# Optimization experiments

Hardware: AMD Instinct MI355X
Metric: run time of the kernel (lower is better)

The kernel has to match this reference:

```python
import jax, jax.numpy as jnp
import numpy as np

B, S, H, I, E, TOP_K, NS = 2, 2048, 2048, 1408, 8, 2, 2
SI = I * NS  # shared expert intermediate (intermediate_size * num_shared_expert)
INIT = 0.02


def setup_inputs() -> dict:
    key = jax.random.key(0)
    ks = jax.random.split(key, 9)
    f32 = jnp.float32
    return {
        "hidden_states": jax.random.normal(ks[0], (B, S, H), f32),
        # router classifier: Linear(H, E, bias=False), torch weight [E, H]
        "router_w": (jax.random.normal(ks[1], (E, H), f32) * INIT),
        # grouped experts (SwiGLU, no bias): [E, H, I], [E, H, I], [E, I, H]
        "gate_w": (jax.random.normal(ks[2], (E, H, I), f32) * INIT),
        "up_w": (jax.random.normal(ks[3], (E, H, I), f32) * INIT),
        "down_w": (jax.random.normal(ks[4], (E, I, H), f32) * INIT),
        # shared expert _MLP (bias=True), stored in matmul orientation
        "s_gate_w": (jax.random.normal(ks[5], (H, SI), f32) * INIT),
        "s_gate_b": jnp.zeros((SI,), f32),
        "s_up_w": (jax.random.normal(ks[6], (H, SI), f32) * INIT),
        "s_up_b": jnp.zeros((SI,), f32),
        "s_down_w": (jax.random.normal(ks[7], (SI, H), f32) * INIT),
        "s_down_b": jnp.zeros((H,), f32),
    }


def reference(hidden_states, router_w, gate_w, up_w, down_w,
              s_gate_w, s_gate_b, s_up_w, s_up_b, s_down_w, s_down_b):
    b, s, h = hidden_states.shape
    x = hidden_states.reshape(-1, h)          # [T, H]
    T = x.shape[0]
    num_experts = router_w.shape[0]

    # ---- router: logits -> fp32 softmax -> top-k -> renormalize ----
    logits = x @ router_w.T                   # [T, E]
    probs = jax.nn.softmax(logits.astype(jnp.float32), axis=-1)
    topk_w, topk_idx = jax.lax.top_k(probs, TOP_K)            # [T, K]
    topk_w = topk_w / jnp.sum(topk_w, axis=-1, keepdims=True)
    # dense combine weights [T, E]; zero for unrouted experts
    combine = jnp.zeros((T, num_experts), probs.dtype)
    combine = combine.at[jnp.arange(T)[:, None], topk_idx].add(topk_w)

    # ---- grouped SwiGLU experts; scan over E keeps peak memory at [T, I] ----
    def expert_step(acc, ws):
        gw, uw, dw, ce = ws                  # [H,I], [H,I], [I,H], [T]
        out = (jax.nn.silu(x @ gw) * (x @ uw)) @ dw           # [T, H]
        return acc + ce[:, None].astype(out.dtype) * out, None

    moe_out, _ = jax.lax.scan(expert_step, jnp.zeros_like(x),
                              (gate_w, up_w, down_w, combine.T))

    # ---- shared expert SwiGLU MLP (bias=True), overlapped -> added ----
    shared = (jax.nn.silu(x @ s_gate_w + s_gate_b)
              * (x @ s_up_w + s_up_b)) @ s_down_w + s_down_b

    return (moe_out + shared).reshape(b, s, h)
```

## Files before the change

### kernel.cpp

```cpp
#include <hip/hip_runtime.h>
#include <hip/hip_bf16.h>
#include <stdint.h>

#define T_TOK 4096
#define HDIM  2048
#define IDIM  1408
#define NEXP  8
#define SIDIM 2816
#define GU_CAP 781
#define DN_CAP 568

typedef __bf16 bf16_t;
typedef __bf16 bf16x8 __attribute__((ext_vector_type(8)));
typedef __bf16 bf16x4 __attribute__((ext_vector_type(4)));
typedef float  f32x4  __attribute__((ext_vector_type(4)));

typedef uint32_t __attribute__((address_space(3))) lds_u32;
typedef uint32_t __attribute__((address_space(1))) glb_u32;

__device__ __forceinline__ void glds16(const bf16_t* g, const char* l) {
  __builtin_amdgcn_global_load_lds((const glb_u32*)g, (lds_u32*)l, 16, 0, 0);
}

__device__ __forceinline__ void bar() {
  asm volatile("" ::: "memory");
  __builtin_amdgcn_s_barrier();
  asm volatile("" ::: "memory");
}
#define VMW4 asm volatile("s_waitcnt vmcnt(4)" ::: "memory")
#define VMW0 asm volatile("s_waitcnt vmcnt(0)" ::: "memory")

__device__ __forceinline__ int xcd_swz(int orig, int nwg) {
  int q = nwg >> 3, r = nwg & 7;
  int x = orig & 7, i = orig >> 3;
  return (x < r ? x * (q + 1) : r * (q + 1) + (x - r) * q) + i;
}

__global__ void tcvt_all_kernel(const float* __restrict__ gate, const float* __restrict__ up,
                                const float* __restrict__ sgw, const float* __restrict__ suw,
                                const float* __restrict__ down, const float* __restrict__ sdw,
                                bf16_t* __restrict__ BguR, bf16_t* __restrict__ BguS,
                                bf16_t* __restrict__ dT, bf16_t* __restrict__ sdT) {
  const int b = blockIdx.x;
  const float* in; bf16_t* out; int R, C, bx, by, which = 0; bool gu;
  if (b < 11264) {
    int z = b / 704, rem = b - z * 704;
    bx = rem % 22; by = rem / 22;
    int e = z >> 1; which = z & 1;
    in = (which ? up : gate) + (size_t)e * HDIM * IDIM;
    out = BguR + (size_t)e * (2 * IDIM) * HDIM;
    R = HDIM; C = IDIM; gu = true;
  } else if (b < 14080) {
    int k = b - 11264;
    int z = k / 1408, rem = k - z * 1408;
    bx = rem % 44; by = rem / 44;
    which = z;
    in = which ? suw : sgw;
    out = BguS;
    R = HDIM; C = SIDIM; gu = true;
  } else if (b < 19712) {
    int k = b - 14080;
    int z = k / 704, rem = k - z * 704;
    bx = rem % 32; by = rem / 32;
    in = down + (size_t)z * IDIM * HDIM;
    out = dT + (size_t)z * HDIM * IDIM;
    R = IDIM; C = HDIM; gu = false;
  } else {
    int k = b - 19712;
    bx = k % 32; by = k / 32;
    in = sdw; out = sdT;
    R = SIDIM; C = HDIM; gu = false;
  }
  __shared__ float tf[64 * 64];
  const int r0 = by * 64, c0 = bx * 64;
  const int tid = threadIdx.x;
  const int cb = tid & 15, rr = tid >> 4;
#pragma unroll
  for (int s = 0; s < 4; ++s) {
    int r = rr + 16 * s;
    float4 v = *(const float4*)(in + (size_t)(r0 + r) * C + c0 + cb * 4);
    int slot = (cb ^ (r & 7) ^ ((r >> 4) << 1)) & 15;
    *(float4*)&tf[r * 64 + slot * 4] = v;
  }
  __syncthreads();
  const int c = tid >> 2, rb = (tid & 3) * 16;
  bf16x8 w0, w1;
#pragma unroll
  for (int i = 0; i < 16; ++i) {
    int r = rb + i;
    int slot = ((c >> 2) ^ (r & 7) ^ ((r >> 4) << 1)) & 15;
    float v = tf[r * 64 + slot * 4 + (c & 3)];
    if (i < 8) w0[i] = (bf16_t)v; else w1[i - 8] = (bf16_t)v;
  }
  int cg = c0 + c;
  int nprime = gu ? (((cg >> 4) << 5) + which * 16 + (cg & 15)) : cg;
  bf16_t* op = out + (size_t)nprime * R + r0 + rb;
  *(bf16x8*)op = w0;
  *(bf16x8*)(op + 8) = w1;
}

__global__ void router_kernel(const float* __restrict__ x, const float* __restrict__ rw,
                              bf16_t* __restrict__ xb,
                              int* __restrict__ tk_i, float* __restrict__ tk_w,
                              int* __restrict__ counts) {
  int gtid = blockIdx.x * 256 + threadIdx.x;
  int t = gtid >> 6, lane = gtid & 63;
  const float4* xr = (const float4*)(x + (size_t)t * HDIM);
  bf16x4* xo = (bf16x4*)(xb + (size_t)t * HDIM);
  float acc[NEXP];
#pragma unroll
  for (int e = 0; e < NEXP; e++) acc[e] = 0.f;
  for (int i = lane; i < HDIM / 4; i += 64) {
    float4 xv = xr[i];
    bf16x4 o;
    o[0] = (bf16_t)xv.x; o[1] = (bf16_t)xv.y; o[2] = (bf16_t)xv.z; o[3] = (bf16_t)xv.w;
    xo[i] = o;
#pragma unroll
    for (int e = 0; e < NEXP; e++) {
      float4 wv = ((const float4*)(rw + e * HDIM))[i];
      acc[e] += xv.x * wv.x + xv.y * wv.y + xv.z * wv.z + xv.w * wv.w;
    }
  }
#pragma unroll
  for (int e = 0; e < NEXP; e++)
#pragma unroll
    for (int off = 32; off; off >>= 1) acc[e] += __shfl_down(acc[e], off);
  if (lane == 0) {
    int i1 = 0; float m1 = acc[0];
#pragma unroll
    for (int e = 1; e < NEXP; e++) if (acc[e] > m1) { m1 = acc[e]; i1 = e; }
    int i2 = -1; float m2 = -1e30f;
#pragma unroll
    for (int e = 0; e < NEXP; e++) if (e != i1 && acc[e] > m2) { m2 = acc[e]; i2 = e; }
    float w1 = 1.f / (1.f + __expf(m2 - m1));
    tk_i[t * 2] = i1; tk_i[t * 2 + 1] = i2;
    tk_w[t * 2] = w1; tk_w[t * 2 + 1] = 1.f - w1;
    atomicAdd(&counts[i1], 1); atomicAdd(&counts[i2], 1);
  }
}

__global__ void build_kernel(int* __restrict__ meta) {
  __shared__ int snmt;
  if (threadIdx.x == 0) {
    int o = 0;
    for (int e = 0; e < NEXP; e++) { meta[16 + e] = o; o += meta[e]; }
    meta[24] = o;
    int nmt = 0;
    for (int e = 0; e < NEXP; e++) {
      int nt = (meta[e] + 255) >> 8;
      for (int i = 0; i < nt; i++) { meta[32 + nmt] = e; meta[80 + nmt] = i << 8; nmt++; }
    }
    meta[25] = nmt;
    meta[26] = nmt * 11 + 352;
    meta[27] = nmt * 8 + 256;
    snmt = nmt;
  }
  __syncthreads();
  const int nmt = snmt;
  int4* gt = (int4*)(meta + 128);
  const int ng = nmt * 11 + 352;
  for (int i = threadIdx.x; i < ng; i += 256) {
    int4 v; v.w = 0;
    if (i < nmt * 11) {
      int g = i / (nmt * 2), rem = i - g * (nmt * 2);
      int yt, xt;
      if (g < 5) { yt = rem >> 1; xt = g * 2 + (rem & 1); }
      else       { yt = rem;      xt = 10; }
      v.x = 0 | (meta[32 + yt] << 1); v.y = meta[80 + yt]; v.z = xt * 256;
    } else {
      int k = i - nmt * 11;
      int g = k >> 5, rem = k & 31;
      int yt = rem >> 1, xt = g * 2 + (rem & 1);
      v.x = 1; v.y = yt * 256; v.z = xt * 256;
    }
    gt[i] = v;
  }
  int4* dt4 = (int4*)(meta + 3328);
  const int nd = nmt * 8 + 256;
  for (int i = threadIdx.x; i < nd; i += 256) {
    int4 v; v.w = 0;
    if (i < nmt * 8) {
      int g = i / (nmt * 2), rem = i - g * (nmt * 2);
      int yt = rem >> 1, xt = g * 2 + (rem & 1);
      v.x = 0 | (meta[32 + yt] << 1); v.y = meta[80 + yt]; v.z = xt * 256;
    } else {
      int k = i - nmt * 8;
      int xt = k >> 5, rem = k & 31, ks = rem >> 4, yt = rem & 15;
      v.x = 1 | (ks << 4); v.y = yt * 256; v.z = xt * 256;
    }
    dt4[i] = v;
  }
}

__global__ void scatter_kernel(const int* __restrict__ tk_i, const float* __restrict__ tk_w,
                               int* __restrict__ meta, int* __restrict__ tok_idx,
                               int* __restrict__ tk_slot) {
  int t = blockIdx.x * 256 + threadIdx.x;
  if (t >= T_TOK) return;
#pragma unroll
  for (int k = 0; k < 2; k++) {
    int e = tk_i[t * 2 + k];
    int pos = meta[16 + e] + atomicAdd(&meta[8 + e], 1);
    tok_idx[pos] = t; tk_slot[t * 2 + k] = pos;
  }
}

template <int OP>
__device__ __forceinline__
void gemm8p_body(const bf16_t* __restrict__ A0, const bf16_t* __restrict__ A1,
                 const bf16_t* __restrict__ B0, const bf16_t* __restrict__ B1,
                 bf16_t* __restrict__ O0, bf16_t* __restrict__ O1, bf16_t* __restrict__ O2,
                 const float* __restrict__ bg, const float* __restrict__ bu,
                 const int* __restrict__ meta, const int* __restrict__ tok_idx) {
  const int ntiles = meta[OP == 0 ? 26 : 27];
  const int l = blockIdx.x;
  if (l >= ntiles) return;
  const int s = xcd_swz(l, ntiles);
  const int4 tv = ((const int4*)(meta + (OP == 0 ? 128 : 3328)))[s];
  const int kind = tv.x & 1, e = (tv.x >> 1) & 7, ks = (tv.x >> 4) & 1;
  const int row0 = tv.y, n0 = tv.z;

  int cnt, slot0 = 0, strideA, strideB, koff = 0;
  const bf16_t *Ab, *Bp;
  constexpr int NKT = (OP == 0) ? (HDIM / 64) : (IDIM / 64);
  if (OP == 0) {
    strideA = HDIM; strideB = HDIM; Ab = A0;
    if (kind == 0) {
      slot0 = meta[16 + e]; cnt = meta[17 + e] - slot0;
      Bp = B0 + (size_t)e * (2 * IDIM) * HDIM;
    } else { cnt = T_TOK; Bp = B1; }
  } else {
    if (kind == 0) {
      slot0 = meta[16 + e]; cnt = meta[17 + e] - slot0;
      Ab = A0; strideA = IDIM;
      Bp = B0 + (size_t)e * HDIM * IDIM; strideB = IDIM;
    } else {
      cnt = T_TOK; Ab = A1; strideA = SIDIM;
      Bp = B1; strideB = SIDIM; koff = ks * IDIM;
    }
  }

  __shared__ __align__(16) char smem[131072];

  const int t = threadIdx.x;
  const int lane = t & 63, wid = t >> 6;
  const int wr = wid >> 2, wc = wid & 3;
  const int lr = lane & 15, lg = lane >> 4;

  const bf16_t* pA[4]; const bf16_t* pB[4]; int dG[4];
#pragma unroll
  for (int j = 0; j < 4; ++j) {
    int g = j * 512 + t;
    int r = g >> 3;
    int c16 = (g & 7) ^ (r & 7);
    dG[j] = g * 16;
    int rr = row0 + r;
    if (kind == 0 && rr >= cnt) rr = cnt - 1;
    int arow;
    if (OP == 0 && kind == 0) arow = tok_idx[slot0 + rr];
    else if (OP == 1 && kind == 0) arow = slot0 + rr;
    else arow = rr;
    pA[j] = Ab + (size_t)arow * strideA + koff + c16 * 8;
    pB[j] = Bp + (size_t)(n0 + r) * strideB + koff + c16 * 8;
  }

  const int cswz0 = ((lg) ^ (lr & 7)) * 16;
  const int cswz1 = ((4 + lg) ^ (lr & 7)) * 16;
  const int aRowB = (wr * 128 + lr) * 128;
  const int bRowB = (wc * 64 + lr) * 128 + 65536;

  f32x4 acc[8][4];
#pragma unroll
  for (int mi = 0; mi < 8; ++mi)
#pragma unroll
    for (int ni = 0; ni < 4; ++ni) acc[mi][ni] = (f32x4)(0.f);

  bf16x8 aL[4][2], aH[4][2], bL[2][2], bH[2][2];

#define ST_A(BUFO, KT, JH) { \
    glds16(pA[(JH)*2]   + (KT)*64, smem + (BUFO) + dG[(JH)*2]); \
    glds16(pA[(JH)*2+1] + (KT)*64, smem + (BUFO) + dG[(JH)*2+1]); }
#define ST_B(BUFO, KT, JH) { \
    glds16(pB[(JH)*2]   + (KT)*64, smem + 65536 + (BUFO) + dG[(JH)*2]); \
    glds16(pB[(JH)*2+1] + (KT)*64, smem + 65536 + (BUFO) + dG[(JH)*2+1]); }
#define RD_A(af, BUFO, MIH) { \
    _Pragma("unroll") for (int mi = 0; mi < 4; ++mi) { \
      af[mi][0] = *(const bf16x8*)(smem + (BUFO) + aRowB + (MIH)*8192 + mi*2048 + cswz0); \
      af[mi][1] = *(const bf16x8*)(smem + (BUFO) + aRowB + (MIH)*8192 + mi*2048 + cswz1); } }
#define RD_B(bf, BUFO, NIH) { \
    _Pragma("unroll") for (int ni = 0; ni < 2; ++ni) { \
      bf[ni][0] = *(const bf16x8*)(smem + (BUFO) + bRowB + (NIH)*4096 + ni*2048 + cswz0); \
      bf[ni][1] = *(const bf16x8*)(smem + (BUFO) + bRowB + (NIH)*4096 + ni*2048 + cswz1); } }
#define MMQ(af, bf, MO, NO) { \
    __builtin_amdgcn_s_setprio(1); \
    _Pragma("unroll") for (int ni = 0; ni < 2; ++ni) \
    _Pragma("unroll") for (int mi = 0; mi < 4; ++mi) { \
      acc[(MO)+mi][(NO)+ni] = __builtin_amdgcn_mfma_f32_16x16x32_bf16(af[mi][0], bf[ni][0], acc[(MO)+mi][(NO)+ni], 0, 0, 0); \
      acc[(MO)+mi][(NO)+ni] = __builtin_amdgcn_mfma_f32_16x16x32_bf16(af[mi][1], bf[ni][1], acc[(MO)+mi][(NO)+ni], 0, 0, 0); } \
    __builtin_amdgcn_s_setprio(0); }
#define KTILE(KT, BO, NBO, W) { \
    RD_A(aL, BO, 0); RD_B(bL, BO, 0); \
    if ((KT) + 1 < NKT) ST_B(NBO, (KT) + 1, 0); \
    bar(); MMQ(aL, bL, 0, 0); bar(); \
    RD_A(aH, BO, 1); \
    if ((KT) + 1 < NKT) ST_B(NBO, (KT) + 1, 1); \
    bar(); MMQ(aH, bL, 4, 0); bar(); \
    RD_B(bH, BO, 1); \
    if ((KT) + 2 < NKT) ST_A(BO, (KT) + 2, 0); \
    bar(); MMQ(aH, bH, 4, 2); bar(); \
    if ((KT) + 2 < NKT) ST_A(BO, (KT) + 2, 1); \
    bar(); MMQ(aL, bH, 0, 2); \
    W; bar(); }

  ST_A(0, 0, 0); ST_A(0, 0, 1);
  ST_B(0, 0, 0); ST_B(0, 0, 1);
  ST_A(32768, 1, 0); ST_A(32768, 1, 1);
  VMW4; bar();

  for (int kt = 0; kt < NKT - 2; kt += 2) {
    KTILE(kt, 0, 32768, VMW4);
    KTILE(kt + 1, 32768, 0, VMW4);
  }
  KTILE(NKT - 2, 0, 32768, VMW0);
  KTILE(NKT - 1, 32768, 0, VMW0);

  if (OP == 0) {
    bf16_t* Ho = kind ? O1 : O0;
    const int HN = kind ? SIDIM : IDIM;
    const int Lbase = n0 >> 1;
#pragma unroll
    for (int mi = 0; mi < 8; ++mi)
#pragma unroll
      for (int j = 0; j < 4; ++j) {
        int row = wr * 128 + mi * 16 + lg * 4 + j;
        int grow = row0 + row;
        if (kind == 0 && grow >= cnt) continue;
        size_t orow = (size_t)((kind ? 0 : slot0) + grow);
#pragma unroll
        for (int nih = 0; nih < 2; ++nih) {
          int Lr = wc * 32 + nih * 16 + lr;
          float g = acc[mi][2 * nih][j];
          float u = acc[mi][2 * nih + 1][j];
          if (kind) { g += bg[Lbase + Lr]; u += bu[Lbase + Lr]; }
          float h = (g / (1.f + __expf(-g))) * u;
          Ho[orow * HN + Lbase + Lr] = (bf16_t)h;
        }
      }
  } else {
    bf16_t* Po = kind ? (ks ? O2 : O1) : O0;
#pragma unroll
    for (int mi = 0; mi < 8; ++mi)
#pragma unroll
      for (int j = 0; j < 4; ++j) {
        int row = wr * 128 + mi * 16 + lg * 4 + j;
        int grow = row0 + row;
        if (kind == 0 && grow >= cnt) continue;
        size_t orow = (size_t)((kind ? 0 : slot0) + grow);
#pragma unroll
        for (int ni = 0; ni < 4; ++ni) {
          int col = n0 + wc * 64 + ni * 16 + lr;
          Po[orow * HDIM + col] = (bf16_t)acc[mi][ni][j];
        }
      }
  }
#undef ST_A
#undef ST_B
#undef RD_A
#undef RD_B
#undef MMQ
#undef KTILE
}

__global__ __launch_bounds__(512, 2)
void gu_gemm(const bf16_t* A0, const bf16_t* A1, const bf16_t* B0, const bf16_t* B1,
             bf16_t* O0, bf16_t* O1, bf16_t* O2, const float* bg, const float* bu,
             const int* meta, const int* tok_idx) {
  gemm8p_body<0>(A0, A1, B0, B1, O0, O1, O2, bg, bu, meta, tok_idx);
}
__global__ __launch_bounds__(512, 2)
void dn_gemm(const bf16_t* A0, const bf16_t* A1, const bf16_t* B0, const bf16_t* B1,
             bf16_t* O0, bf16_t* O1, bf16_t* O2, const float* bg, const float* bu,
             const int* meta, const int* tok_idx) {
  gemm8p_body<1>(A0, A1, B0, B1, O0, O1, O2, bg, bu, meta, tok_idx);
}

__global__ void combine_kernel(const bf16_t* __restrict__ sh0, const bf16_t* __restrict__ sh1,
                               const bf16_t* __restrict__ rt, const int* __restrict__ tk_slot,
                               const float* __restrict__ tk_w, const float* __restrict__ sdb,
                               float* __restrict__ out) {
  const int t = blockIdx.x;
  const int c = threadIdx.x * 8;
  const int s1 = tk_slot[2 * t], s2 = tk_slot[2 * t + 1];
  const float w1 = tk_w[2 * t], w2 = tk_w[2 * t + 1];
  bf16x8 a = *(const bf16x8*)(sh0 + (size_t)t * HDIM + c);
  bf16x8 b = *(const bf16x8*)(sh1 + (size_t)t * HDIM + c);
  bf16x8 r1 = *(const bf16x8*)(rt + (size_t)s1 * HDIM + c);
  bf16x8 r2 = *(const bf16x8*)(rt + (size_t)s2 * HDIM + c);
  float4 d0 = *(const float4*)(sdb + c);
  float4 d1 = *(const float4*)(sdb + c + 4);
  float o[8];
#pragma unroll
  for (int i = 0; i < 8; i++)
    o[i] = (float)a[i] + (float)b[i] + w1 * (float)r1[i] + w2 * (float)r2[i];
  o[0] += d0.x; o[1] += d0.y; o[2] += d0.z; o[3] += d0.w;
  o[4] += d1.x; o[5] += d1.y; o[6] += d1.z; o[7] += d1.w;
  float4* op = (float4*)(out + (size_t)t * HDIM + c);
  op[0] = make_float4(o[0], o[1], o[2], o[3]);
  op[1] = make_float4(o[4], o[5], o[6], o[7]);
}

extern "C" void kernel_launch(void* const* d_in, const int* in_sizes, int n_in,
                              void* d_out, int out_size, void* d_ws, size_t ws_size,
                              hipStream_t stream) {
  const float* x_f  = (const float*)d_in[0];
  const float* rw   = (const float*)d_in[1];
  const float* gate = (const float*)d_in[2];
  const float* up   = (const float*)d_in[3];
  const float* down = (const float*)d_in[4];
  const float* sgw  = (const float*)d_in[5];
  const float* sgb  = (const float*)d_in[6];
  const float* suw  = (const float*)d_in[7];
  const float* sub  = (const float*)d_in[8];
  const float* sdw  = (const float*)d_in[9];
  const float* sdb  = (const float*)d_in[10];
  float* out = (float*)d_out;

  char* ws = (char*)d_ws;
  size_t off = 0;
  auto alloc = [&](size_t bytes) {
    char* p = ws + off;
    off += (bytes + 255) & ~(size_t)255;
    return p;
  };
  bf16_t* xb    = (bf16_t*)alloc((size_t)T_TOK * HDIM * 2);
  char*   bgur  = alloc((size_t)NEXP * 2 * IDIM * HDIM * 2);
  bf16_t* BguR  = (bf16_t*)bgur;
  bf16_t* BguS  = (bf16_t*)alloc((size_t)2 * SIDIM * HDIM * 2);
  bf16_t* dT    = (bf16_t*)alloc((size_t)NEXP * HDIM * IDIM * 2);
  bf16_t* sdT   = (bf16_t*)alloc((size_t)HDIM * SIDIM * 2);
  bf16_t* hid_r = (bf16_t*)alloc((size_t)(T_TOK * 2) * IDIM * 2);
  bf16_t* hid_s = (bf16_t*)alloc((size_t)T_TOK * SIDIM * 2);
  int*    meta  = (int*)alloc(32768);
  int*    tok_idx = (int*)alloc(8192 * 4);
  int*    tk_slot = (int*)alloc(8192 * 4);
  int*    tk_i    = (int*)alloc((size_t)T_TOK * 2 * 4);
  float*  tk_w2   = (float*)alloc((size_t)T_TOK * 2 * 4);

  bf16_t* rt_p  = (bf16_t*)bgur;
  bf16_t* sh_p0 = (bf16_t*)(bgur + (size_t)8192 * HDIM * 2);
  bf16_t* sh_p1 = (bf16_t*)(bgur + (size_t)8192 * HDIM * 2 + (size_t)T_TOK * HDIM * 2);

  hipMemsetAsync(meta, 0, 64, stream);

  tcvt_all_kernel<<<21120, 256, 0, stream>>>(
      gate, up, sgw, suw, down, sdw, BguR, BguS, dT, sdT);

  router_kernel<<<T_TOK / 4, 256, 0, stream>>>(x_f, rw, xb, tk_i, tk_w2, meta);
  build_kernel<<<1, 256, 0, stream>>>(meta);
  scatter_kernel<<<T_TOK / 256, 256, 0, stream>>>(tk_i, tk_w2, meta, tok_idx, tk_slot);

  gu_gemm<<<GU_CAP, 512, 0, stream>>>(
      xb, nullptr, BguR, BguS, hid_r, hid_s, nullptr, sgb, sub, meta, tok_idx);
  dn_gemm<<<DN_CAP, 512, 0, stream>>>(
      hid_r, hid_s, dT, sdT, rt_p, sh_p0, sh_p1, nullptr, nullptr, meta, nullptr);
  combine_kernel<<<T_TOK, 256, 0, stream>>>(sh_p0, sh_p1, rt_p, tk_slot, tk_w2, sdb, out);
}
```

Measured before the change: 588.3 us.

## Drop build kernel; derive tile schedule from expert counts inside GEMM and scatter kernels

Removes the single-block build_kernel launch. Each GEMM block now recomputes per-expert offsets and tile counts from the raw counts and decodes its own tile descriptor, and scatter computes prefix offsets in shared memory. This saves one serialized launch and the table writes and reads, in exchange for a little redundant scalar work per block. It also adds an lgkmcnt(8) wait before the first barrier in the K-tile loop to order the LDS reads.

Result: faster. 567.9 us (-3.5%).

```diff
diff --git a/kernel.cpp b/kernel.cpp
--- a/kernel.cpp
+++ b/kernel.cpp
@@ -29,6 +29,7 @@
 }
 #define VMW4 asm volatile("s_waitcnt vmcnt(4)" ::: "memory")
 #define VMW0 asm volatile("s_waitcnt vmcnt(0)" ::: "memory")
+#define LGK8 asm volatile("s_waitcnt lgkmcnt(8)" ::: "memory")
 
 __device__ __forceinline__ int xcd_swz(int orig, int nwg) {
   int q = nwg >> 3, r = nwg & 7;
@@ -139,68 +140,25 @@
   }
 }
 
-__global__ void build_kernel(int* __restrict__ meta) {
-  __shared__ int snmt;
-  if (threadIdx.x == 0) {
-    int o = 0;
-    for (int e = 0; e < NEXP; e++) { meta[16 + e] = o; o += meta[e]; }
-    meta[24] = o;
-    int nmt = 0;
-    for (int e = 0; e < NEXP; e++) {
-      int nt = (meta[e] + 255) >> 8;
-      for (int i = 0; i < nt; i++) { meta[32 + nmt] = e; meta[80 + nmt] = i << 8; nmt++; }
-    }
-    meta[25] = nmt;
-    meta[26] = nmt * 11 + 352;
-    meta[27] = nmt * 8 + 256;
-    snmt = nmt;
-  }
-  __syncthreads();
-  const int nmt = snmt;
-  int4* gt = (int4*)(meta + 128);
-  const int ng = nmt * 11 + 352;
-  for (int i = threadIdx.x; i < ng; i += 256) {
-    int4 v; v.w = 0;
-    if (i < nmt * 11) {
-      int g = i / (nmt * 2), rem = i - g * (nmt * 2);
-      int yt, xt;
-      if (g < 5) { yt = rem >> 1; xt = g * 2 + (rem & 1); }
-      else       { yt = rem;      xt = 10; }
-      v.x = 0 | (meta[32 + yt] << 1); v.y = meta[80 + yt]; v.z = xt * 256;
-    } else {
-      int k = i - nmt * 11;
-      int g = k >> 5, rem = k & 31;
-      int yt = rem >> 1, xt = g * 2 + (rem & 1);
-      v.x = 1; v.y = yt * 256; v.z = xt * 256;
-    }
-    gt[i] = v;
-  }
-  int4* dt4 = (int4*)(meta + 3328);
-  const int nd = nmt * 8 + 256;
-  for (int i = threadIdx.x; i < nd; i += 256) {
-    int4 v; v.w = 0;
-    if (i < nmt * 8) {
-      int g = i / (nmt * 2), rem = i - g * (nmt * 2);
-      int yt = rem >> 1, xt = g * 2 + (rem & 1);
-      v.x = 0 | (meta[32 + yt] << 1); v.y = meta[80 + yt]; v.z = xt * 256;
-    } else {
-      int k = i - nmt * 8;
-      int xt = k >> 5, rem = k & 31, ks = rem >> 4, yt = rem & 15;
-      v.x = 1 | (ks << 4); v.y = yt * 256; v.z = xt * 256;
-    }
-    dt4[i] = v;
-  }
-}
-
-__global__ void scatter_kernel(const int* __restrict__ tk_i, const float* __restrict__ tk_w,
+__global__ void scatter_kernel(const int* __restrict__ tk_i,
                                int* __restrict__ meta, int* __restrict__ tok_idx,
                                int* __restrict__ tk_slot) {
+  __shared__ int offs[NEXP];
+  if (threadIdx.x < NEXP) {
+    int o = 0;
+#pragma unroll
+    for (int i = 0; i < NEXP; ++i) { if (i == threadIdx.x) break; o += meta[i]; }
+    o = 0;
+    for (int i = 0; i < (int)threadIdx.x; ++i) o += meta[i];
+    offs[threadIdx.x] = o;
+  }
+  __syncthreads();
   int t = blockIdx.x * 256 + threadIdx.x;
   if (t >= T_TOK) return;
 #pragma unroll
   for (int k = 0; k < 2; k++) {
     int e = tk_i[t * 2 + k];
-    int pos = meta[16 + e] + atomicAdd(&meta[8 + e], 1);
+    int pos = offs[e] + atomicAdd(&meta[8 + e], 1);
     tok_idx[pos] = t; tk_slot[t * 2 + k] = pos;
   }
 }
@@ -212,13 +170,53 @@
                  bf16_t* __restrict__ O0, bf16_t* __restrict__ O1, bf16_t* __restrict__ O2,
                  const float* __restrict__ bg, const float* __restrict__ bu,
                  const int* __restrict__ meta, const int* __restrict__ tok_idx) {
-  const int ntiles = meta[OP == 0 ? 26 : 27];
+  int nt[NEXP], offp[NEXP];
+  int nmt = 0, osum = 0;
+#pragma unroll
+  for (int i = 0; i < NEXP; ++i) {
+    offp[i] = osum; osum += meta[i];
+    nt[i] = (meta[i] + 255) >> 8;
+    nmt += nt[i];
+  }
+  const int ntiles = (OP == 0) ? (nmt * 11 + 352) : (nmt * 8 + 256);
   const int l = blockIdx.x;
   if (l >= ntiles) return;
   const int s = xcd_swz(l, ntiles);
-  const int4 tv = ((const int4*)(meta + (OP == 0 ? 128 : 3328)))[s];
-  const int kind = tv.x & 1, e = (tv.x >> 1) & 7, ks = (tv.x >> 4) & 1;
-  const int row0 = tv.y, n0 = tv.z;
+
+  int kind, e = 0, row0, n0, ks = 0;
+  if (OP == 0) {
+    if (s < nmt * 11) {
+      kind = 0;
+      int g = s / (nmt * 2), rem = s - g * (nmt * 2);
+      int yt, xt;
+      if (g < 5) { yt = rem >> 1; xt = g * 2 + (rem & 1); }
+      else       { yt = rem;      xt = 10; }
+      int acc = 0, ytin = 0;
+#pragma unroll
+      for (int i = 0; i < NEXP; ++i) { if (yt >= acc) { e = i; ytin = yt - acc; } acc += nt[i]; }
+      row0 = ytin << 8; n0 = xt * 256;
+    } else {
+      kind = 1;
+      int k = s - nmt * 11, g = k >> 5, rem = k & 31;
+      row0 = (rem >> 1) * 256; n0 = (g * 2 + (rem & 1)) * 256;
+    }
+  } else {
+    if (s < nmt * 8) {
+      kind = 0;
+      int g = s / (nmt * 2), rem = s - g * (nmt * 2);
+      int yt = rem >> 1, xt = g * 2 + (rem & 1);
+      int acc = 0, ytin = 0;
+#pragma unroll
+      for (int i = 0; i < NEXP; ++i) { if (yt >= acc) { e = i; ytin = yt - acc; } acc += nt[i]; }
+      row0 = ytin << 8; n0 = xt * 256;
+    } else {
+      kind = 1;
+      int k = s - nmt * 8;
+      int xt = k >> 5, rem = k & 31;
+      ks = rem >> 4;
+      row0 = (rem & 15) * 256; n0 = xt * 256;
+    }
+  }
 
   int cnt, slot0 = 0, strideA, strideB, koff = 0;
   const bf16_t *Ab, *Bp;
@@ -226,12 +224,12 @@
   if (OP == 0) {
     strideA = HDIM; strideB = HDIM; Ab = A0;
     if (kind == 0) {
-      slot0 = meta[16 + e]; cnt = meta[17 + e] - slot0;
+      slot0 = offp[e]; cnt = meta[e];
       Bp = B0 + (size_t)e * (2 * IDIM) * HDIM;
     } else { cnt = T_TOK; Bp = B1; }
   } else {
     if (kind == 0) {
-      slot0 = meta[16 + e]; cnt = meta[17 + e] - slot0;
+      slot0 = offp[e]; cnt = meta[e];
       Ab = A0; strideA = IDIM;
       Bp = B0 + (size_t)e * HDIM * IDIM; strideB = IDIM;
     } else {
@@ -301,6 +299,7 @@
 #define KTILE(KT, BO, NBO, W) { \
     RD_A(aL, BO, 0); RD_B(bL, BO, 0); \
     if ((KT) + 1 < NKT) ST_B(NBO, (KT) + 1, 0); \
+    LGK8; \
     bar(); MMQ(aL, bL, 0, 0); bar(); \
     RD_A(aH, BO, 1); \
     if ((KT) + 1 < NKT) ST_B(NBO, (KT) + 1, 1); \
@@ -440,7 +439,7 @@
   bf16_t* sdT   = (bf16_t*)alloc((size_t)HDIM * SIDIM * 2);
   bf16_t* hid_r = (bf16_t*)alloc((size_t)(T_TOK * 2) * IDIM * 2);
   bf16_t* hid_s = (bf16_t*)alloc((size_t)T_TOK * SIDIM * 2);
-  int*    meta  = (int*)alloc(32768);
+  int*    meta  = (int*)alloc(1024);
   int*    tok_idx = (int*)alloc(8192 * 4);
   int*    tk_slot = (int*)alloc(8192 * 4);
   int*    tk_i    = (int*)alloc((size_t)T_TOK * 2 * 4);
@@ -456,8 +455,7 @@
       gate, up, sgw, suw, down, sdw, BguR, BguS, dT, sdT);
 
   router_kernel<<<T_TOK / 4, 256, 0, stream>>>(x_f, rw, xb, tk_i, tk_w2, meta);
-  build_kernel<<<1, 256, 0, stream>>>(meta);
-  scatter_kernel<<<T_TOK / 256, 256, 0, stream>>>(tk_i, tk_w2, meta, tok_idx, tk_slot);
+  scatter_kernel<<<T_TOK / 256, 256, 0, stream>>>(tk_i, meta, tok_idx, tk_slot);
 
   gu_gemm<<<GU_CAP, 512, 0, stream>>>(
       xb, nullptr, BguR, BguS, hid_r, hid_s, nullptr, sgb, sub, meta, tok_idx);
```
